# Kernel optimization log

Hardware: AMD Instinct MI355X
Metric: run time of the kernel (lower is better)

The kernel has to match this reference:

```python
import jax, jax.numpy as jnp
import numpy as np

B, T, D = 4, 2048, 1024
H, KD, VD = 16, 64, 64  # num_heads, key_dim, value_dim; H*KD == D


def setup_inputs() -> dict:
    key = jax.random.key(0)
    ks = jax.random.split(key, 10)
    s = 0.02
    return {
        "q_in": jax.random.normal(ks[0], (B, T, D), jnp.float32),
        "v_in": jax.random.normal(ks[1], (B, T, D), jnp.float32),
        "Wq": jax.random.normal(ks[2], (D, H * KD), jnp.float32) * s,
        "bq": jnp.zeros((H * KD,), jnp.float32),
        "Wk": jax.random.normal(ks[3], (D, H * KD), jnp.float32) * s,
        "bk": jnp.zeros((H * KD,), jnp.float32),
        "Wv": jax.random.normal(ks[4], (D, H * VD), jnp.float32) * s,
        "bv": jnp.zeros((H * VD,), jnp.float32),
        "Wo": jax.random.normal(ks[5], (H * VD, D), jnp.float32) * s,
        "bo": jnp.zeros((D,), jnp.float32),
    }


def reference(q_in, v_in, Wq, bq, Wk, bk, Wv, bv, Wo, bo):
    # QKV projections (key defaults to value input)
    q = q_in @ Wq + bq                      # [B,T,H*KD]
    k = v_in @ Wk + bk                      # [B,T,H*KD]
    v = v_in @ Wv + bv                      # [B,T,H*VD]
    q = q.reshape(B, T, H, KD)
    k = k.reshape(B, T, H, KD)
    v = v.reshape(B, T, H, VD)
    # scaled dot-product attention, scores materialized as [B,H,Tq,Tv]
    q = q / jnp.sqrt(jnp.asarray(KD, q.dtype))
    scores = jnp.einsum('bqnh,bvnh->bnqv', q, k)
    weights = jax.nn.softmax(scores, axis=-1)
    out = jnp.einsum('bnqv,bvnh->bqnh', weights, v)  # [B,Tq,H,VD]
    out = out.reshape(B, T, H * VD)
    return out @ Wo + bo                    # [B,T,D]
```

## Files before the change

kernel.cpp:

```cpp
#include <hip/hip_runtime.h>

#define BATCH  4
#define T_SEQ  2048
#define NH     16
#define DMODEL 1024
#define HD     64

typedef float    f32x4 __attribute__((ext_vector_type(4)));
typedef _Float16 f16x8 __attribute__((ext_vector_type(8)));
typedef _Float16 f16x4 __attribute__((ext_vector_type(4)));
typedef __fp16   h16x2 __attribute__((ext_vector_type(2)));

#define LOG2E 1.44269504088896f

__device__ __forceinline__ void lds_load16(const void* g, void* l) {
  __builtin_amdgcn_global_load_lds((const __attribute__((address_space(1))) void*)g,
                                   (__attribute__((address_space(3))) void*)l, 16, 0, 0);
}

__device__ __forceinline__ f16x4 pack4_f16(float a, float b, float c, float d) {
  union { h16x2 h[2]; f16x4 f; } u;
  u.h[0] = __builtin_amdgcn_cvt_pkrtz(a, b);
  u.h[1] = __builtin_amdgcn_cvt_pkrtz(c, d);
  return u.f;
}

#define MEMFENCE asm volatile("" ::: "memory")
#define WAITVM4  asm volatile("s_waitcnt vmcnt(4)" ::: "memory")
#define WAITVM0  asm volatile("s_waitcnt vmcnt(0)" ::: "memory")
#define PH_ENTER do { MEMFENCE; __builtin_amdgcn_s_barrier(); \
                      asm volatile("s_waitcnt lgkmcnt(0)" ::: "memory"); } while (0)
#define PH_EXIT  do { MEMFENCE; __builtin_amdgcn_s_barrier(); MEMFENCE; } while (0)

__global__ __launch_bounds__(256) void cast2_f32_to_f16(
    const float* __restrict__ a, const float* __restrict__ bsrc,
    _Float16* __restrict__ oa, _Float16* __restrict__ ob, int n4) {
  const float* in = blockIdx.y ? bsrc : a;
  _Float16* out = blockIdx.y ? ob : oa;
  int i = blockIdx.x * 256 + threadIdx.x;
  if (i < n4) {
    float4 v = ((const float4*)in)[i];
    f16x4 o = { (_Float16)v.x, (_Float16)v.y, (_Float16)v.z, (_Float16)v.w };
    ((f16x4*)out)[i] = o;
  }
}

__global__ __launch_bounds__(256) void transcast_w4(
    const float* __restrict__ W0, const float* __restrict__ W1,
    const float* __restrict__ W2, const float* __restrict__ W3,
    _Float16* __restrict__ T0, _Float16* __restrict__ T1,
    _Float16* __restrict__ T2, _Float16* __restrict__ T3) {
  const float* W; _Float16* Wt;
  switch (blockIdx.z) {
    case 0: W = W0; Wt = T0; break;
    case 1: W = W1; Wt = T1; break;
    case 2: W = W2; Wt = T2; break;
    default: W = W3; Wt = T3; break;
  }
  __shared__ float L[64][65];
  const int n0 = blockIdx.x * 64, k0 = blockIdx.y * 64;
  const int tx = threadIdx.x & 15, ty = threadIdx.x >> 4;
#pragma unroll
  for (int i = 0; i < 4; ++i) {
    float4 v = *(const float4*)&W[(size_t)(k0 + ty + 16 * i) * DMODEL + n0 + tx * 4];
    L[ty + 16 * i][tx * 4 + 0] = v.x;
    L[ty + 16 * i][tx * 4 + 1] = v.y;
    L[ty + 16 * i][tx * 4 + 2] = v.z;
    L[ty + 16 * i][tx * 4 + 3] = v.w;
  }
  __syncthreads();
#pragma unroll
  for (int i = 0; i < 4; ++i) {
    int n = n0 + ty + 16 * i;
    f16x4 o;
#pragma unroll
    for (int j = 0; j < 4; ++j) o[j] = (_Float16)L[tx * 4 + j][ty + 16 * i];
    *(f16x4*)&Wt[(size_t)n * DMODEL + k0 + tx * 4] = o;
  }
}

__device__ __forceinline__ void gemm256_body(
    const _Float16* __restrict__ A, const _Float16* __restrict__ Wt,
    const float* __restrict__ bias, void* __restrict__ Cout, float scale,
    int mode, _Float16* As0, _Float16* Bs0, _Float16* As1, _Float16* Bs1) {
  const int K = DMODEL;
  const int lane = threadIdx.x & 63, wave = threadIdx.x >> 6;
  const int m16 = lane & 15, quad = lane >> 4;
  const int wm = wave & 1;
  const int wn = wave >> 1;

  const int lin = blockIdx.x + blockIdx.y * gridDim.x;
  const int wg = (lin & 7) * 16 + (lin >> 3);
  const int m0 = (wg >> 2) * 256;
  const int n0 = (wg & 3) * 256;

  const int kof = (wave & 1) * 32 + quad * 8;
  const _Float16* aB[2][2]; const _Float16* bB[2][2];
#pragma unroll
  for (int h = 0; h < 2; ++h)
#pragma unroll
    for (int j = 0; j < 2; ++j) {
      int r = h * 128 + (wave >> 1) * 16 + 64 * j + m16;
      aB[h][j] = A  + (size_t)(m0 + r) * K + kof;
      bB[h][j] = Wt + (size_t)(n0 + r) * K + kof;
    }

  auto stageA = [&](_Float16* Ab, int h, int t) {
#pragma unroll
    for (int j = 0; j < 2; ++j)
      lds_load16(aB[h][j] + t * 64, Ab + (h * 16 + wave + 8 * j) * 512);
  };
  auto stageB = [&](_Float16* Bb, int h, int t) {
#pragma unroll
    for (int j = 0; j < 2; ++j)
      lds_load16(bB[h][j] + t * 64, Bb + (h * 16 + wave + 8 * j) * 512);
  };
  auto rdA = [&](const _Float16* Ab, int mi, int kh) {
    return *(const f16x8*)(Ab + (((wm * 8 + mi) * 2 + kh) * 64 + lane) * 8);
  };
  auto rdB = [&](const _Float16* Bb, int ni, int kh) {
    return *(const f16x8*)(Bb + (((wn * 4 + ni) * 2 + kh) * 64 + lane) * 8);
  };

  f32x4 acc[8][4] = {};

  auto tile_step = [&](int t, _Float16* Ac, const _Float16* Bc, _Float16* Bn) {
    f16x8 a03[4][2], a47[4][2], b01[2][2], b23[2][2];
#pragma unroll
    for (int mi = 0; mi < 4; ++mi) { a03[mi][0] = rdA(Ac, mi, 0); a03[mi][1] = rdA(Ac, mi, 1); }
#pragma unroll
    for (int ni = 0; ni < 2; ++ni) { b01[ni][0] = rdB(Bc, ni, 0); b01[ni][1] = rdB(Bc, ni, 1); }
    if (t < 15) stageB(Bn, 0, t + 1);
    PH_ENTER;
    __builtin_amdgcn_s_setprio(1);
#pragma unroll
    for (int mi = 0; mi < 4; ++mi)
#pragma unroll
      for (int ni = 0; ni < 2; ++ni)
#pragma unroll
        for (int kh = 0; kh < 2; ++kh)
          acc[mi][ni] = __builtin_amdgcn_mfma_f32_16x16x32_f16(a03[mi][kh], b01[ni][kh], acc[mi][ni], 0, 0, 0);
    __builtin_amdgcn_s_setprio(0);
    PH_EXIT;
#pragma unroll
    for (int ni = 0; ni < 2; ++ni) { b23[ni][0] = rdB(Bc, 2 + ni, 0); b23[ni][1] = rdB(Bc, 2 + ni, 1); }
    if (t < 15) stageB(Bn, 1, t + 1);
    PH_ENTER;
    __builtin_amdgcn_s_setprio(1);
#pragma unroll
    for (int mi = 0; mi < 4; ++mi)
#pragma unroll
      for (int ni = 0; ni < 2; ++ni)
#pragma unroll
        for (int kh = 0; kh < 2; ++kh)
          acc[mi][2 + ni] = __builtin_amdgcn_mfma_f32_16x16x32_f16(a03[mi][kh], b23[ni][kh], acc[mi][2 + ni], 0, 0, 0);
    __builtin_amdgcn_s_setprio(0);
    PH_EXIT;
#pragma unroll
    for (int mi = 0; mi < 4; ++mi) { a47[mi][0] = rdA(Ac, 4 + mi, 0); a47[mi][1] = rdA(Ac, 4 + mi, 1); }
    PH_ENTER;
    __builtin_amdgcn_s_setprio(1);
#pragma unroll
    for (int mi = 0; mi < 4; ++mi)
#pragma unroll
      for (int ni = 0; ni < 2; ++ni)
#pragma unroll
        for (int kh = 0; kh < 2; ++kh)
          acc[4 + mi][ni] = __builtin_amdgcn_mfma_f32_16x16x32_f16(a47[mi][kh], b01[ni][kh], acc[4 + mi][ni], 0, 0, 0);
    __builtin_amdgcn_s_setprio(0);
    PH_EXIT;
    if (t < 14) { stageA(Ac, 0, t + 2); stageA(Ac, 1, t + 2); }
    PH_ENTER;
    __builtin_amdgcn_s_setprio(1);
#pragma unroll
    for (int mi = 0; mi < 4; ++mi)
#pragma unroll
      for (int ni = 0; ni < 2; ++ni)
#pragma unroll
        for (int kh = 0; kh < 2; ++kh)
          acc[4 + mi][2 + ni] = __builtin_amdgcn_mfma_f32_16x16x32_f16(a47[mi][kh], b23[ni][kh], acc[4 + mi][2 + ni], 0, 0, 0);
    __builtin_amdgcn_s_setprio(0);
    if (t < 14)       WAITVM4;
    else if (t == 14) WAITVM0;
    MEMFENCE; __builtin_amdgcn_s_barrier(); MEMFENCE;
  };

  stageA(As0, 0, 0); stageA(As0, 1, 0);
  stageB(Bs0, 0, 0); stageB(Bs0, 1, 0);
  stageA(As1, 0, 1); stageA(As1, 1, 1);
  WAITVM4;
  MEMFENCE; __builtin_amdgcn_s_barrier(); MEMFENCE;

  for (int tp = 0; tp < 8; ++tp) {
    tile_step(2 * tp,     As0, Bs0, Bs1);
    tile_step(2 * tp + 1, As1, Bs1, Bs0);
  }

  float bv[4];
#pragma unroll
  for (int ni = 0; ni < 4; ++ni) bv[ni] = bias[n0 + wn * 64 + ni * 16 + m16];

  if (mode == 2) {
#pragma unroll
    for (int mi = 0; mi < 8; ++mi)
#pragma unroll
      for (int ni = 0; ni < 4; ++ni) {
        int row = m0 + wm * 128 + mi * 16 + quad * 4;
        int col = n0 + wn * 64 + ni * 16 + m16;
        int bb = row >> 11, tt = row & (T_SEQ - 1);
        int hh = col >> 6, dd = col & 63;
        f16x4 pv = pack4_f16(acc[mi][ni][0] + bv[ni], acc[mi][ni][1] + bv[ni],
                             acc[mi][ni][2] + bv[ni], acc[mi][ni][3] + bv[ni]);
        *(f16x4*)&((_Float16*)Cout)[(((size_t)bb * NH + hh) * HD + dd) * T_SEQ + tt] = pv;
      }
  } else if (mode == 0) {
#pragma unroll
    for (int mi = 0; mi < 8; ++mi)
#pragma unroll
      for (int r = 0; r < 4; ++r) {
        int row = m0 + wm * 128 + mi * 16 + quad * 4 + r;
#pragma unroll
        for (int ni = 0; ni < 4; ++ni) {
          int col = n0 + wn * 64 + ni * 16 + m16;
          float v = (acc[mi][ni][r] + bv[ni]) * scale;
          ((_Float16*)Cout)[(size_t)row * DMODEL + col] = (_Float16)v;
        }
      }
  } else {
#pragma unroll
    for (int mi = 0; mi < 8; ++mi)
#pragma unroll
      for (int r = 0; r < 4; ++r) {
        int row = m0 + wm * 128 + mi * 16 + quad * 4 + r;
#pragma unroll
        for (int ni = 0; ni < 4; ++ni) {
          int col = n0 + wn * 64 + ni * 16 + m16;
          ((float*)Cout)[(size_t)row * DMODEL + col] = acc[mi][ni][r] + bv[ni];
        }
      }
  }
}

__global__ __launch_bounds__(512, 2) void gemm_qkv(
    const _Float16* __restrict__ Aq, const _Float16* __restrict__ Av,
    const _Float16* __restrict__ Wq, const _Float16* __restrict__ Wk,
    const _Float16* __restrict__ Wv,
    const float* __restrict__ bq, const float* __restrict__ bk,
    const float* __restrict__ bv,
    _Float16* __restrict__ Cq, _Float16* __restrict__ Ck, _Float16* __restrict__ Cv) {
  __shared__ _Float16 As[2][16384], Bs[2][16384];
  const _Float16* A; const _Float16* Wt; const float* bias; _Float16* C;
  float scale; int mode;
  if (blockIdx.z == 0)      { A = Aq; Wt = Wq; bias = bq; C = Cq; scale = 0.125f * LOG2E; mode = 0; }
  else if (blockIdx.z == 1) { A = Av; Wt = Wk; bias = bk; C = Ck; scale = 1.f; mode = 0; }
  else                      { A = Av; Wt = Wv; bias = bv; C = Cv; scale = 1.f; mode = 2; }
  gemm256_body(A, Wt, bias, C, scale, mode, As[0], Bs[0], As[1], Bs[1]);
}

__global__ __launch_bounds__(256, 3) void gemm_out(
    const _Float16* __restrict__ A, const _Float16* __restrict__ Wt,
    const float* __restrict__ bias, float* __restrict__ Cout) {
  __shared__ _Float16 As[128 * 64], Bs[128 * 64];
  const int K = DMODEL;
  const int lane = threadIdx.x & 63, wave = threadIdx.x >> 6;
  const int bid = blockIdx.x + blockIdx.y * gridDim.x;
  const int m0 = ((bid & 7) * 8 + ((bid >> 3) & 7)) * 128;
  const int n0 = (bid >> 6) * 128;
  const int wr = (wave & 1) * 4, wc = (wave >> 1) * 4;
  const int m16 = lane & 15, quad = lane >> 4;

  const _Float16* ap[4]; const _Float16* bp[4];
#pragma unroll
  for (int j = 0; j < 4; ++j) {
    int g = wave * 4 + j;
    ap[j] = A  + (size_t)(m0 + (g >> 1) * 16 + m16) * K + (g & 1) * 32 + quad * 8;
    bp[j] = Wt + (size_t)(n0 + (g >> 1) * 16 + m16) * K + (g & 1) * 32 + quad * 8;
  }

  f32x4 acc[4][4] = {};

  for (int k0 = 0; k0 < 1024; k0 += 64) {
    __syncthreads();
#pragma unroll
    for (int j = 0; j < 4; ++j) {
      lds_load16(ap[j] + k0, As + (wave * 4 + j) * 512);
      lds_load16(bp[j] + k0, Bs + (wave * 4 + j) * 512);
    }
    __syncthreads();
#pragma unroll
    for (int s = 0; s < 2; ++s) {
      f16x8 bf[4];
#pragma unroll
      for (int ni = 0; ni < 4; ++ni)
        bf[ni] = *(const f16x8*)(Bs + (((wc + ni) * 2 + s) * 64 + lane) * 8);
#pragma unroll
      for (int mi = 0; mi < 4; ++mi) {
        f16x8 af = *(const f16x8*)(As + (((wr + mi) * 2 + s) * 64 + lane) * 8);
#pragma unroll
        for (int ni = 0; ni < 4; ++ni)
          acc[mi][ni] = __builtin_amdgcn_mfma_f32_16x16x32_f16(af, bf[ni], acc[mi][ni], 0, 0, 0);
      }
    }
  }

#pragma unroll
  for (int mi = 0; mi < 4; ++mi)
#pragma unroll
    for (int r = 0; r < 4; ++r) {
      int row = m0 + (wr + mi) * 16 + quad * 4 + r;
#pragma unroll
      for (int ni = 0; ni < 4; ++ni) {
        int col = n0 + (wc + ni) * 16 + m16;
        Cout[(size_t)row * DMODEL + col] = acc[mi][ni][r] + bias[col];
      }
    }
}

__global__ __launch_bounds__(256, 2) void attn_mfma(
    const _Float16* __restrict__ Q, const _Float16* __restrict__ Kb,
    const _Float16* __restrict__ Vt, _Float16* __restrict__ O) {
  __shared__ _Float16 Ks[2][64 * 64], Vs[2][64 * 64];
  __shared__ _Float16 Ps[4 * 4096];

  const int lane = threadIdx.x & 63, wave = threadIdx.x >> 6;
  const int m16 = lane & 15, quad = lane >> 4;
  const int h = blockIdx.x;
  const int q0 = blockIdx.y * 256;
  const int b = blockIdx.z;
  const int wq = wave * 64;
  const int wbase = wave * 4096;

  f16x8 qf[4][2];
#pragma unroll
  for (int mi = 0; mi < 4; ++mi)
#pragma unroll
    for (int ki = 0; ki < 2; ++ki) {
      int q = q0 + wq + mi * 16 + m16;
      qf[mi][ki] = *(const f16x8*)(Q + (((size_t)b * T_SEQ + q) * NH + h) * HD + ki * 32 + quad * 8);
    }

  const _Float16 *kp[2], *vp[2];
#pragma unroll
  for (int i = 0; i < 2; ++i) {
    int g = wave * 128 + i * 64 + lane;
    int tk = (g >> 7) * 16 + (g & 15);
    int dkof = ((g >> 6) & 1) * 32 + ((g >> 4) & 3) * 8;
    kp[i] = Kb + (((size_t)b * T_SEQ + tk) * NH + h) * HD + dkof;
    int dvof = (g >> 7) * 16 + (g & 15);
    int tv = ((g >> 6) & 1) * 32 + ((g >> 4) & 3) * 8;
    vp[i] = Vt + (((size_t)b * NH + h) * HD + dvof) * T_SEQ + tv;
  }

  auto stageKV = [&](int c, int kv) {
#pragma unroll
    for (int i = 0; i < 2; ++i) {
      lds_load16(kp[i] + (size_t)kv * (NH * HD), Ks[c] + (wave * 2 + i) * 512);
      lds_load16(vp[i] + kv, Vs[c] + (wave * 2 + i) * 512);
    }
  };

  int pw[4][4];
#pragma unroll
  for (int mi = 0; mi < 4; ++mi)
#pragma unroll
    for (int nt = 0; nt < 4; ++nt) {
      int kt = nt >> 1;
      int q8 = ((nt & 1) << 1) | (quad >> 1);
      pw[mi][nt] = wbase + ((mi * 2 + kt) * 64 + q8 * 16 + m16) * 8 + (quad & 1) * 4;
    }

  const f16x8 onef = {(_Float16)1, (_Float16)1, (_Float16)1, (_Float16)1,
                      (_Float16)1, (_Float16)1, (_Float16)1, (_Float16)1};

  f32x4 o_acc[4][4] = {};
  f32x4 l_acc[4] = {};

  stageKV(0, 0);
  WAITVM0;
  MEMFENCE; __builtin_amdgcn_s_barrier(); MEMFENCE;

  for (int t = 0; t < 32; ++t) {
    const int c = t & 1;
    if (t < 31) stageKV(c ^ 1, (t + 1) * 64);

    f32x4 st[4][4] = {};
#pragma unroll
    for (int nt = 0; nt < 4; ++nt)
#pragma unroll
      for (int ki = 0; ki < 2; ++ki) {
        f16x8 kf = *(const f16x8*)(Ks[c] + ((nt * 2 + ki) * 64 + lane) * 8);
        __builtin_amdgcn_s_setprio(1);
#pragma unroll
        for (int mi = 0; mi < 4; ++mi)
          st[mi][nt] = __builtin_amdgcn_mfma_f32_16x16x32_f16(kf, qf[mi][ki], st[mi][nt], 0, 0, 0);
        __builtin_amdgcn_s_setprio(0);
      }

#pragma unroll
    for (int mi = 0; mi < 4; ++mi)
#pragma unroll
      for (int nt = 0; nt < 4; ++nt) {
        f16x4 p = pack4_f16(__builtin_amdgcn_exp2f(st[mi][nt][0]),
                            __builtin_amdgcn_exp2f(st[mi][nt][1]),
                            __builtin_amdgcn_exp2f(st[mi][nt][2]),
                            __builtin_amdgcn_exp2f(st[mi][nt][3]));
        *(f16x4*)(Ps + pw[mi][nt]) = p;
      }

#pragma unroll
    for (int kt = 0; kt < 2; ++kt) {
      f16x8 pf[4];
#pragma unroll
      for (int mi = 0; mi < 4; ++mi) {
        pf[mi] = *(const f16x8*)(Ps + wbase + ((mi * 2 + kt) * 64 + lane) * 8);
        l_acc[mi] = __builtin_amdgcn_mfma_f32_16x16x32_f16(pf[mi], onef, l_acc[mi], 0, 0, 0);
      }
#pragma unroll
      for (int nd = 0; nd < 4; ++nd) {
        f16x8 vf = *(const f16x8*)(Vs[c] + ((nd * 2 + kt) * 64 + lane) * 8);
        __builtin_amdgcn_s_setprio(1);
#pragma unroll
        for (int mi = 0; mi < 4; ++mi)
          o_acc[mi][nd] = __builtin_amdgcn_mfma_f32_16x16x32_f16(pf[mi], vf, o_acc[mi][nd], 0, 0, 0);
        __builtin_amdgcn_s_setprio(0);
      }
    }

    WAITVM0;
    MEMFENCE; __builtin_amdgcn_s_barrier(); MEMFENCE;
  }

#pragma unroll
  for (int mi = 0; mi < 4; ++mi)
#pragma unroll
    for (int r = 0; r < 4; ++r) {
      float inv = 1.f / l_acc[mi][r];
      int q = q0 + wq + mi * 16 + quad * 4 + r;
#pragma unroll
      for (int nd = 0; nd < 4; ++nd) {
        int d = nd * 16 + m16;
        O[(((size_t)b * T_SEQ + q) * NH + h) * HD + d] = (_Float16)(o_acc[mi][nd][r] * inv);
      }
    }
}

extern "C" void kernel_launch(void* const* d_in, const int* in_sizes, int n_in,
                              void* d_out, int out_size, void* d_ws, size_t ws_size,
                              hipStream_t stream) {
  const float* q_in = (const float*)d_in[0];
  const float* v_in = (const float*)d_in[1];
  const float* Wq   = (const float*)d_in[2];
  const float* bq   = (const float*)d_in[3];
  const float* Wk   = (const float*)d_in[4];
  const float* bk   = (const float*)d_in[5];
  const float* Wv   = (const float*)d_in[6];
  const float* bv   = (const float*)d_in[7];
  const float* Wo   = (const float*)d_in[8];
  const float* bo   = (const float*)d_in[9];
  float* out = (float*)d_out;

  const size_t MB = 1u << 20;
  char* ws = (char*)d_ws;
  _Float16* q16  = (_Float16*)(ws);
  _Float16* v16  = (_Float16*)(ws + 16 * MB);
  _Float16* qbuf = (_Float16*)(ws + 32 * MB);
  _Float16* kbuf = (_Float16*)(ws + 48 * MB);
  _Float16* vtb  = (_Float16*)(ws + 64 * MB);
  _Float16* Wqt  = (_Float16*)(ws + 80 * MB);
  _Float16* Wkt  = (_Float16*)(ws + 82 * MB);
  _Float16* Wvt  = (_Float16*)(ws + 84 * MB);
  _Float16* Wot  = (_Float16*)(ws + 86 * MB);

  const int n4 = BATCH * T_SEQ * DMODEL / 4;
  cast2_f32_to_f16<<<dim3(n4 / 256, 2), 256, 0, stream>>>(q_in, v_in, q16, v16, n4);

  transcast_w4<<<dim3(16, 16, 4), 256, 0, stream>>>(Wq, Wk, Wv, Wo, Wqt, Wkt, Wvt, Wot);

  gemm_qkv<<<dim3(4, 32, 3), 512, 0, stream>>>(q16, v16, Wqt, Wkt, Wvt, bq, bk, bv,
                                               qbuf, kbuf, vtb);

  attn_mfma<<<dim3(16, 8, 4), 256, 0, stream>>>(qbuf, kbuf, vtb, qbuf);

  gemm_out<<<dim3(8, 64), 256, 0, stream>>>(qbuf, Wot, bo, out);
}
```

Before: 331.6 us.

## Merge prep kernels and replace LDS P round-trip with cross-lane shuffles

Two independent changes. The activation cast kernel and the weight transpose-cast kernel are merged into a single launch that dispatches by block index, removing one kernel launch. In attention, the softmax probability tile is no longer written to and re-read from LDS; instead lanes swap half-fragments with an xor-16 shuffle, and the V fragment load uses a permuted lane index to match the new k ordering. This frees LDS (which may raise occupancy) and removes LDS store/load traffic, at the cost of extra shuffle (ds_bpermute-style) instructions and register pressure.

```diff
diff --git a/kernel.cpp b/kernel.cpp
--- a/kernel.cpp
+++ b/kernel.cpp
@@ -22,6 +22,14 @@
   union { h16x2 h[2]; f16x4 f; } u;
   u.h[0] = __builtin_amdgcn_cvt_pkrtz(a, b);
   u.h[1] = __builtin_amdgcn_cvt_pkrtz(c, d);
+  return u.f;
+}
+
+__device__ __forceinline__ f16x4 shflx16(f16x4 v) {
+  union { f16x4 f; int i[2]; } u;
+  u.f = v;
+  u.i[0] = __shfl_xor(u.i[0], 16, 64);
+  u.i[1] = __shfl_xor(u.i[1], 16, 64);
   return u.f;
 }
 
@@ -32,33 +40,33 @@
                       asm volatile("s_waitcnt lgkmcnt(0)" ::: "memory"); } while (0)
 #define PH_EXIT  do { MEMFENCE; __builtin_amdgcn_s_barrier(); MEMFENCE; } while (0)
 
-__global__ __launch_bounds__(256) void cast2_f32_to_f16(
-    const float* __restrict__ a, const float* __restrict__ bsrc,
-    _Float16* __restrict__ oa, _Float16* __restrict__ ob, int n4) {
-  const float* in = blockIdx.y ? bsrc : a;
-  _Float16* out = blockIdx.y ? ob : oa;
-  int i = blockIdx.x * 256 + threadIdx.x;
-  if (i < n4) {
-    float4 v = ((const float4*)in)[i];
-    f16x4 o = { (_Float16)v.x, (_Float16)v.y, (_Float16)v.z, (_Float16)v.w };
-    ((f16x4*)out)[i] = o;
-  }
-}
-
-__global__ __launch_bounds__(256) void transcast_w4(
+__global__ __launch_bounds__(256) void prep(
+    const float* __restrict__ q_in, const float* __restrict__ v_in,
+    _Float16* __restrict__ q16, _Float16* __restrict__ v16,
     const float* __restrict__ W0, const float* __restrict__ W1,
     const float* __restrict__ W2, const float* __restrict__ W3,
     _Float16* __restrict__ T0, _Float16* __restrict__ T1,
     _Float16* __restrict__ T2, _Float16* __restrict__ T3) {
+  __shared__ float L[64][65];
+  const int bid = blockIdx.x;
+  if (bid < 16384) {
+    const float* in = (bid >> 13) ? v_in : q_in;
+    _Float16* out = (bid >> 13) ? v16 : q16;
+    int i = (bid & 8191) * 256 + threadIdx.x;
+    float4 v = ((const float4*)in)[i];
+    f16x4 o = { (_Float16)v.x, (_Float16)v.y, (_Float16)v.z, (_Float16)v.w };
+    ((f16x4*)out)[i] = o;
+    return;
+  }
+  const int wb = bid - 16384;
   const float* W; _Float16* Wt;
-  switch (blockIdx.z) {
+  switch (wb >> 8) {
     case 0: W = W0; Wt = T0; break;
     case 1: W = W1; Wt = T1; break;
     case 2: W = W2; Wt = T2; break;
     default: W = W3; Wt = T3; break;
   }
-  __shared__ float L[64][65];
-  const int n0 = blockIdx.x * 64, k0 = blockIdx.y * 64;
+  const int n0 = ((wb >> 4) & 15) * 64, k0 = (wb & 15) * 64;
   const int tx = threadIdx.x & 15, ty = threadIdx.x >> 4;
 #pragma unroll
   for (int i = 0; i < 4; ++i) {
@@ -320,15 +328,15 @@
     const _Float16* __restrict__ Q, const _Float16* __restrict__ Kb,
     const _Float16* __restrict__ Vt, _Float16* __restrict__ O) {
   __shared__ _Float16 Ks[2][64 * 64], Vs[2][64 * 64];
-  __shared__ _Float16 Ps[4 * 4096];
 
   const int lane = threadIdx.x & 63, wave = threadIdx.x >> 6;
   const int m16 = lane & 15, quad = lane >> 4;
+  const int pe = quad & 1;
+  const int vlane = m16 | ((((quad & 1) << 1) | (quad >> 1)) << 4);
   const int h = blockIdx.x;
   const int q0 = blockIdx.y * 256;
   const int b = blockIdx.z;
   const int wq = wave * 64;
-  const int wbase = wave * 4096;
 
   f16x8 qf[4][2];
 #pragma unroll
@@ -359,16 +367,6 @@
     }
   };
 
-  int pw[4][4];
-#pragma unroll
-  for (int mi = 0; mi < 4; ++mi)
-#pragma unroll
-    for (int nt = 0; nt < 4; ++nt) {
-      int kt = nt >> 1;
-      int q8 = ((nt & 1) << 1) | (quad >> 1);
-      pw[mi][nt] = wbase + ((mi * 2 + kt) * 64 + q8 * 16 + m16) * 8 + (quad & 1) * 4;
-    }
-
   const f16x8 onef = {(_Float16)1, (_Float16)1, (_Float16)1, (_Float16)1,
                       (_Float16)1, (_Float16)1, (_Float16)1, (_Float16)1};
 
@@ -396,28 +394,33 @@
         __builtin_amdgcn_s_setprio(0);
       }
 
+    f16x4 pex[4][4];
 #pragma unroll
     for (int mi = 0; mi < 4; ++mi)
 #pragma unroll
-      for (int nt = 0; nt < 4; ++nt) {
-        f16x4 p = pack4_f16(__builtin_amdgcn_exp2f(st[mi][nt][0]),
-                            __builtin_amdgcn_exp2f(st[mi][nt][1]),
-                            __builtin_amdgcn_exp2f(st[mi][nt][2]),
-                            __builtin_amdgcn_exp2f(st[mi][nt][3]));
-        *(f16x4*)(Ps + pw[mi][nt]) = p;
-      }
+      for (int nt = 0; nt < 4; ++nt)
+        pex[mi][nt] = pack4_f16(__builtin_amdgcn_exp2f(st[mi][nt][0]),
+                                __builtin_amdgcn_exp2f(st[mi][nt][1]),
+                                __builtin_amdgcn_exp2f(st[mi][nt][2]),
+                                __builtin_amdgcn_exp2f(st[mi][nt][3]));
 
 #pragma unroll
     for (int kt = 0; kt < 2; ++kt) {
       f16x8 pf[4];
 #pragma unroll
       for (int mi = 0; mi < 4; ++mi) {
-        pf[mi] = *(const f16x8*)(Ps + wbase + ((mi * 2 + kt) * 64 + lane) * 8);
+        f16x4 Aa = pex[mi][2 * kt], Bb = pex[mi][2 * kt + 1];
+        f16x4 send = pe ? Aa : Bb;
+        f16x4 recv = shflx16(send);
+        union { f16x4 h[2]; f16x8 w; } u;
+        u.h[0] = pe ? recv : Aa;
+        u.h[1] = pe ? Bb : recv;
+        pf[mi] = u.w;
         l_acc[mi] = __builtin_amdgcn_mfma_f32_16x16x32_f16(pf[mi], onef, l_acc[mi], 0, 0, 0);
       }
 #pragma unroll
       for (int nd = 0; nd < 4; ++nd) {
-        f16x8 vf = *(const f16x8*)(Vs[c] + ((nd * 2 + kt) * 64 + lane) * 8);
+        f16x8 vf = *(const f16x8*)(Vs[c] + ((nd * 2 + kt) * 64 + vlane) * 8);
         __builtin_amdgcn_s_setprio(1);
 #pragma unroll
         for (int mi = 0; mi < 4; ++mi)
@@ -471,10 +474,8 @@
   _Float16* Wvt  = (_Float16*)(ws + 84 * MB);
   _Float16* Wot  = (_Float16*)(ws + 86 * MB);
 
-  const int n4 = BATCH * T_SEQ * DMODEL / 4;
-  cast2_f32_to_f16<<<dim3(n4 / 256, 2), 256, 0, stream>>>(q_in, v_in, q16, v16, n4);
-
-  transcast_w4<<<dim3(16, 16, 4), 256, 0, stream>>>(Wq, Wk, Wv, Wo, Wqt, Wkt, Wvt, Wot);
+  prep<<<dim3(16384 + 1024), 256, 0, stream>>>(q_in, v_in, q16, v16,
+                                               Wq, Wk, Wv, Wo, Wqt, Wkt, Wvt, Wot);
 
   gemm_qkv<<<dim3(4, 32, 3), 512, 0, stream>>>(q16, v16, Wqt, Wkt, Wvt, bq, bk, bv,
                                                qbuf, kbuf, vtb);
```

Result: no change. 337.3 us (+1.7%).
